# Performance work log

Measured on AMD Instinct MI355X. Metric: run time of the kernel, lower is better.

The kernel has to match this reference:

```python
import jax, jax.numpy as jnp
import numpy as np

B, N, C, H = 8, 2048, 256, 4
RES = 2048
OUT_C = 1


def _split_heads(t, h):
    b, n, hd = t.shape
    return t.reshape(b, n, h, hd // h).transpose(0, 2, 1, 3)


def _merge_heads(t):
    b, h, n, d = t.shape
    return t.transpose(0, 2, 1, 3).reshape(b, n, h * d)


def _inst_norm(x, eps=1e-5):
    # torch InstanceNorm1d applied per-token over head dim, no affine, biased var
    mu = jnp.mean(x, -1, keepdims=True)
    var = jnp.mean((x - mu) ** 2, -1, keepdims=True)
    return (x - mu) / jnp.sqrt(var + eps)


def _layer_norm(x, g, b, eps=1e-5):
    mu = jnp.mean(x, -1, keepdims=True)
    var = jnp.mean((x - mu) ** 2, -1, keepdims=True)
    return (x - mu) / jnp.sqrt(var + eps) * g + b


def _rot_half(x):
    d = x.shape[-1] // 2
    return jnp.concatenate([-x[..., d:], x[..., :d]], axis=-1)


def _rotary_freqs(coords, dim, mult):
    # RotaryEmbedding: t * (scale/min_freq), outer with inv_freq, cat(f, f)
    inv = 1.0 / (10000.0 ** (jnp.arange(0, dim, 2, dtype=jnp.float32) / dim))
    f = (coords * mult)[..., None] * inv  # [..., dim//2]
    return jnp.concatenate([f, f], axis=-1)


def _apply_rot(t, f):
    return t * jnp.cos(f) + _rot_half(t) * jnp.sin(f)


def _gelu(x):
    return jax.nn.gelu(x, approximate=False)


def setup_inputs():
    key = jax.random.key(0)
    ks = jax.random.split(key, 20)
    def rn(k, shp, s=0.02):
        return jax.random.normal(k, shp, dtype=jnp.float32) * s
    return {
        "z": jax.random.normal(ks[0], (B, N, C), jnp.float32),
        "propagate_pos": jax.random.uniform(ks[1], (B, N, 1), jnp.float32),
        # Gaussian Fourier feature matrix (fixed, scale=8)
        "B_fourier": jax.random.normal(ks[2], (1, C), jnp.float32) * 8.0,
        "W_coord": rn(ks[3], (2 * C, C)),
        # CrossLinearAttention (heads=4, dim_head=C, project_query=False)
        "W_kv": rn(ks[4], (C, 2 * H * C)),
        "Wo_ca": rn(ks[5], (H * C, C)),
        "bo_ca": jnp.zeros((C,), jnp.float32),
        # CrossFormer FFN (mlp_dim=C)
        "Wf1": rn(ks[6], (C, C)), "bf1": jnp.zeros((C,), jnp.float32),
        "Wf2": rn(ks[7], (C, C)), "bf2": jnp.zeros((C,), jnp.float32),
        # propagator: LayerNorm + 3-layer GELU MLP (no biases)
        "ln_g": jnp.ones((C,), jnp.float32), "ln_b": jnp.zeros((C,), jnp.float32),
        "P1": rn(ks[8], (C + 1, C)), "P2": rn(ks[9], (C, C)), "P3": rn(ks[10], (C, C)),
        # decode LinearAttention (heads=1, dim_head=C)
        "W_qkv": rn(ks[11], (C, 3 * C)),
        "Wo_da": rn(ks[12], (C, C)), "bo_da": jnp.zeros((C,), jnp.float32),
        # decode FFN
        "ln2_g": jnp.ones((C,), jnp.float32), "ln2_b": jnp.zeros((C,), jnp.float32),
        "D1": rn(ks[13], (C, C)), "D2": rn(ks[14], (C, C // 2)),
        "D3": rn(ks[15], (C // 2, OUT_C)), "b3": jnp.zeros((OUT_C,), jnp.float32),
    }


def reference(z, propagate_pos, B_fourier, W_coord, W_kv, Wo_ca, bo_ca,
              Wf1, bf1, Wf2, bf2, ln_g, ln_b, P1, P2, P3,
              W_qkv, Wo_da, bo_da, ln2_g, ln2_b, D1, D2, D3, b3):
    pos = propagate_pos  # [B, N, 1]
    n = z.shape[1]
    # --- coordinate projection: Gaussian Fourier features -> GELU -> Linear ---
    xp = 2.0 * np.pi * ((pos / 16.0) @ B_fourier)            # [B, N, C]
    feat = jnp.concatenate([jnp.sin(xp), jnp.cos(xp)], -1)   # [B, N, 2C]
    x = _gelu(feat) @ W_coord                                # [B, N, C]
    # --- cross linear attention ('fourier', heads=4, dim_head=C, q unprojected) ---
    k, v = jnp.split(z @ W_kv, 2, axis=-1)
    k = _split_heads(k, H)
    v = _split_heads(v, H)                                   # [B, H, N, C]
    q = jnp.broadcast_to(x[:, None], (x.shape[0], H, n, C))  # repeat query over heads
    q = _inst_norm(q)
    k = _inst_norm(k)
    f = _rotary_freqs(pos[..., 0], C, float(RES))[:, None]   # scale/min_freq = res
    q = _apply_rot(q, f)
    k = _apply_rot(k, f)                                     # z_pos=None -> same freqs
    dots = jnp.einsum('bhnd,bhne->bhde', k, v)               # [B, H, C, C]
    out = jnp.einsum('bhnd,bhde->bhne', q, dots) / n
    x = _merge_heads(out) @ Wo_ca + bo_ca + x
    # --- CrossFormer FFN + residual ---
    x = _gelu(x @ Wf1 + bf1) @ Wf2 + bf2 + x
    # --- propagator: LN, concat(pos/16), 3-layer GELU MLP, residual ---
    h = jnp.concatenate([_layer_norm(x, ln_g, ln_b), pos / 16.0], -1)
    zp = _gelu(_gelu(h @ P1) @ P2) @ P3 + x
    # --- decode: linear self-attention (heads=1, fourier) + FFN ---
    q2, k2, v2 = jnp.split(zp @ W_qkv, 3, axis=-1)           # each [B, N, C]
    q2 = _inst_norm(q2)
    k2 = _inst_norm(k2)
    f2 = _rotary_freqs(pos[..., 0], C, float(RES))
    q2 = _apply_rot(q2, f2)
    k2 = _apply_rot(k2, f2)
    dots2 = jnp.einsum('bnd,bne->bde', k2, v2)               # [B, C, C]
    att = jnp.einsum('bnd,bde->bne', q2, dots2) / n
    zd = att @ Wo_da + bo_da + zp
    h2 = _layer_norm(zd, ln2_g, ln2_b)
    u = _gelu(_gelu(h2 @ D1) @ D2) @ D3 + b3                 # [B, N, OUT_C]
    u = jnp.transpose(u, (0, 2, 1))                          # 'b n (t c) -> b (t c) n', t=1
    return (u, zp)
```

## Files before the change

kernel.cpp:

```cpp
#include <hip/hip_runtime.h>
#include <hip/hip_bf16.h>

using bf16 = __hip_bfloat16;
typedef __attribute__((ext_vector_type(8))) short short8;
typedef __attribute__((ext_vector_type(4))) short short4v;
typedef __attribute__((ext_vector_type(4))) float f32x4;

constexpr int BB = 8;
constexpr int NN = 2048;
constexpr int CC = 256;
constexpr int NTOK = BB * NN;
constexpr float TWO_PI = 6.283185307179586f;
constexpr float LOG2_1E4 = 13.287712379549449f;

__device__ __forceinline__ float gelu_f(float x) {
  return 0.5f * x * (1.0f + erff(x * 0.7071067811865475f));
}

template <int T>
__device__ __forceinline__ void stats_rows(const float (*buf)[CC], float* mu, float* rs, float eps) {
  __syncthreads();
  int w = threadIdx.x >> 6, l = threadIdx.x & 63;
  if (w < T) {
    float s = 0.f, s2 = 0.f;
#pragma unroll
    for (int j = 0; j < 4; ++j) { float v = buf[w][l + 64 * j]; s += v; s2 += v * v; }
#pragma unroll
    for (int o = 32; o; o >>= 1) { s += __shfl_down(s, o); s2 += __shfl_down(s2, o); }
    if (l == 0) {
      float m = s * (1.f / 256.f);
      float var = fmaxf(s2 * (1.f / 256.f) - m * m, 0.f);
      mu[w] = m; rs[w] = rsqrtf(var + eps);
    }
  }
  __syncthreads();
}

#define GLD16(src, dst)                                                       \
  __builtin_amdgcn_global_load_lds(                                           \
      (const __attribute__((address_space(1))) void*)(src),                   \
      (__attribute__((address_space(3))) void*)(dst), 16, 0, 0)

template <int K, int MI>
__device__ __forceinline__ void gemm_core(
    const bf16* __restrict__ Ap, int lda, const bf16* __restrict__ Bp,
    bf16 (&As)[MI * 32 * 64], bf16 (&Bs)[64 * 64], f32x4 (&acc)[MI][2]) {
  const int tid = threadIdx.x;
  const int w = tid >> 6, l = tid & 63;
  const int srow = l >> 3, scol = (l & 7) * 8;
  const int wm = w >> 1, wn = w & 1;
  for (int kt = 0; kt < K; kt += 64) {
#pragma unroll
    for (int i = 0; i < MI; ++i) {
      int r = (w * MI + i) * 8 + srow;
      GLD16(Ap + (long)r * lda + kt + scol, &As[(w * MI + i) * 512 + l * 8]);
    }
#pragma unroll
    for (int i = 0; i < 2; ++i) {
      int r = (w * 2 + i) * 8 + srow;
      GLD16(Bp + (long)r * K + kt + scol, &Bs[(w * 2 + i) * 512 + l * 8]);
    }
    __syncthreads();
    short8 bfr[2][2];
#pragma unroll
    for (int ni = 0; ni < 2; ++ni)
#pragma unroll
      for (int ks = 0; ks < 2; ++ks)
        bfr[ni][ks] = *(const short8*)&Bs[(wn * 32 + ni * 16 + (l & 15)) * 64 + ks * 32 + (l >> 4) * 8];
#pragma unroll
    for (int mi = 0; mi < MI; ++mi) {
#pragma unroll
      for (int ks = 0; ks < 2; ++ks) {
        short8 afr = *(const short8*)&As[(wm * (MI * 16) + mi * 16 + (l & 15)) * 64 + ks * 32 + (l >> 4) * 8];
#pragma unroll
        for (int ni = 0; ni < 2; ++ni)
          acc[mi][ni] = __builtin_amdgcn_mfma_f32_16x16x32_bf16(afr, bfr[ni][ks], acc[mi][ni], 0, 0, 0);
      }
    }
    __syncthreads();
  }
}

enum { E_BF16 = 0, E_BIAS_RESB_BOTH, E_BIAS_GELU, E_BIAS_RES_F32,
       E_RANK1_GELU, E_GELU, E_RES_BOTH };

template <int K, int EPI>
__global__ void __launch_bounds__(256) k_gemm(
    const bf16* __restrict__ A, int lda, const bf16* __restrict__ Bt,
    long bstride, long zstride, int nOffZ,
    const float* __restrict__ bias, const float* __restrict__ res,
    const bf16* __restrict__ resB, const float* __restrict__ rank1,
    const float* __restrict__ pvec,
    float* __restrict__ outF, bf16* __restrict__ outB, int ldo) {
  __shared__ bf16 As[128 * 64];
  __shared__ bf16 Bs[64 * 64];
  const int tid = threadIdx.x;
  const int w = tid >> 6, l = tid & 63;
  const int m0 = blockIdx.y * 128, n0 = blockIdx.x * 64;
  const int bidx = m0 >> 11;
  const bf16* Bp = Bt + (long)bidx * bstride + (long)blockIdx.z * zstride + (long)n0 * K;
  f32x4 acc[4][2] = {};
  gemm_core<K, 4>(A + (long)m0 * lda, lda, Bp, As, Bs, acc);
  const int wm = w >> 1, wn = w & 1;
  const int zoff = blockIdx.z * nOffZ;
#pragma unroll
  for (int mi = 0; mi < 4; ++mi) {
#pragma unroll
    for (int ni = 0; ni < 2; ++ni) {
      const int bcol = n0 + wn * 32 + ni * 16 + (l & 15);
      const int ocol = bcol + zoff;
#pragma unroll
      for (int r = 0; r < 4; ++r) {
        const int row = m0 + wm * 64 + mi * 16 + (l >> 4) * 4 + r;
        float v = acc[mi][ni][r];
        const long oidx = (long)row * ldo + ocol;
        if constexpr (EPI == E_BF16) { outB[oidx] = __float2bfloat16(v); }
        else if constexpr (EPI == E_BIAS_RESB_BOTH) {
          v += bias[bcol] + __bfloat162float(resB[oidx]);
          outF[oidx] = v; outB[oidx] = __float2bfloat16(v);
        } else if constexpr (EPI == E_BIAS_GELU) {
          v = gelu_f(v + bias[bcol]); outB[oidx] = __float2bfloat16(v);
        } else if constexpr (EPI == E_BIAS_RES_F32) {
          v += bias[bcol] + res[oidx]; outF[oidx] = v;
        } else if constexpr (EPI == E_RANK1_GELU) {
          v = gelu_f(v + pvec[row] * rank1[bcol]); outB[oidx] = __float2bfloat16(v);
        } else if constexpr (EPI == E_GELU) {
          v = gelu_f(v); outB[oidx] = __float2bfloat16(v);
        } else {
          v += res[oidx]; outF[oidx] = v; outB[oidx] = __float2bfloat16(v);
        }
      }
    }
  }
}

template <int K>
__global__ void __launch_bounds__(256) k_gemmT(
    const bf16* __restrict__ A, int lda, const bf16* __restrict__ Bt,
    bf16* __restrict__ T0, bf16* __restrict__ T1, int thresh, int matsPerB,
    float* __restrict__ sS, float* __restrict__ sS2) {
  __shared__ union {
    struct { bf16 A[128 * 64]; bf16 B[64 * 64]; } ab;
    bf16 stage[64 * 132];
  } sm;
  const int tid = threadIdx.x;
  const int w = tid >> 6, l = tid & 63;
  const int m0 = blockIdx.y * 128, n0 = blockIdx.x * 64;
  f32x4 acc[4][2] = {};
  gemm_core<K, 4>(A + (long)m0 * lda, lda, Bt + (long)n0 * K, sm.ab.A, sm.ab.B, acc);
  const int wm = w >> 1, wn = w & 1;

  if (n0 < thresh) {
    float sr[16], s2r[16];
#pragma unroll
    for (int mi = 0; mi < 4; ++mi)
#pragma unroll
      for (int r = 0; r < 4; ++r) {
        float v0 = acc[mi][0][r], v1 = acc[mi][1][r];
        sr[mi * 4 + r] = v0 + v1;
        s2r[mi * 4 + r] = v0 * v0 + v1 * v1;
      }
#pragma unroll
    for (int o = 1; o < 16; o <<= 1) {
#pragma unroll
      for (int i = 0; i < 16; ++i) {
        sr[i] += __shfl_xor(sr[i], o);
        s2r[i] += __shfl_xor(s2r[i], o);
      }
    }
    if ((l & 15) == 0) {
      const int head = n0 >> 8;
      const long base = (long)head * 16384 + m0 + wm * 64 + (l >> 4) * 4;
#pragma unroll
      for (int mi = 0; mi < 4; ++mi)
#pragma unroll
        for (int r = 0; r < 4; ++r) {
          atomicAdd(&sS[base + mi * 16 + r], sr[mi * 4 + r]);
          atomicAdd(&sS2[base + mi * 16 + r], s2r[mi * 4 + r]);
        }
    }
  }

#pragma unroll
  for (int mi = 0; mi < 4; ++mi)
#pragma unroll
    for (int ni = 0; ni < 2; ++ni) {
      int c = wn * 32 + ni * 16 + (l & 15);
      int row0 = wm * 64 + mi * 16 + (l >> 4) * 4;
#pragma unroll
      for (int q = 0; q < 2; ++q) {
        bf16 b0 = __float2bfloat16(acc[mi][ni][2 * q]);
        bf16 b1 = __float2bfloat16(acc[mi][ni][2 * q + 1]);
        unsigned u = (unsigned)*(unsigned short*)&b0 |
                     ((unsigned)*(unsigned short*)&b1 << 16);
        *(unsigned*)&sm.stage[c * 132 + row0 + 2 * q] = u;
      }
    }
  __syncthreads();
  const int b = m0 >> 11, nbase = m0 & 2047;
  const int part = (n0 >= thresh) ? 1 : 0;
  const int cT0 = n0 - (part ? thresh : 0);
  bf16* dst = (part ? T1 : T0) + ((long)(b * matsPerB + (cT0 >> 8))) * 524288
            + (long)(cT0 & 255) * 2048;
  const int c = tid >> 2, ns = tid & 3;
  bf16* rowp = dst + (long)c * 2048 + nbase + ns * 32;
#pragma unroll
  for (int j = 0; j < 4; ++j) {
    short4v lo = *(const short4v*)&sm.stage[c * 132 + ns * 32 + j * 8];
    short4v hi = *(const short4v*)&sm.stage[c * 132 + ns * 32 + j * 8 + 4];
    short8 v;
    v[0] = lo[0]; v[1] = lo[1]; v[2] = lo[2]; v[3] = lo[3];
    v[4] = hi[0]; v[5] = hi[1]; v[6] = hi[2]; v[7] = hi[3];
    *(short8*)&rowp[j * 8] = v;
  }
}

template <int MI>
__global__ void __launch_bounds__(256) k_atb2(
    const bf16* __restrict__ A0, const bf16* __restrict__ B0,
    bf16* __restrict__ D0, float scale) {
  __shared__ bf16 As[MI * 32 * 64];
  __shared__ bf16 Bs[64 * 64];
  const int tid = threadIdx.x;
  const int w = tid >> 6, l = tid & 63;
  const int mat = blockIdx.z;
  const int m0 = blockIdx.y * (MI * 32), n0 = blockIdx.x * 64;
  const bf16* Ap = A0 + (long)mat * 524288 + (long)m0 * 2048;
  const bf16* Bp = B0 + (long)mat * 524288 + (long)n0 * 2048;
  f32x4 acc[MI][2] = {};
  gemm_core<2048, MI>(Ap, 2048, Bp, As, Bs, acc);
  bf16* D = D0 + (long)mat * 65536;
  const int wm = w >> 1, wn = w & 1;
#pragma unroll
  for (int mi = 0; mi < MI; ++mi)
#pragma unroll
    for (int ni = 0; ni < 2; ++ni) {
      int col = n0 + wn * 32 + ni * 16 + (l & 15);
#pragma unroll
      for (int r = 0; r < 4; ++r) {
        int row = m0 + wm * (MI * 16) + mi * 16 + (l >> 4) * 4 + r;
        D[(long)row * 256 + col] = __float2bfloat16(acc[mi][ni][r] * scale);
      }
    }
}

__global__ void __launch_bounds__(256) k_rotnorm(
    bf16* __restrict__ Kt, const float* __restrict__ sS, const float* __restrict__ sS2,
    const bf16* __restrict__ csT, int hshift) {
  const int mat = blockIdx.y, c = blockIdx.x;
  const int n = threadIdx.x * 8;
  const int b = mat >> hshift, h = mat & ((1 << hshift) - 1);
  bf16* r0 = Kt + (long)mat * 524288 + (long)c * 2048 + n;
  bf16* r1 = r0 + 128 * 2048;
  const long tok = (long)b * 2048 + n;
  const bf16* cop = csT + ((long)c * 2) * 16384 + tok;
  const bf16* sip = cop + 16384;
  const float* sp = sS + (long)h * 16384 + tok;
  const float* s2p = sS2 + (long)h * 16384 + tok;
  short8 v0 = *(const short8*)r0, v1 = *(const short8*)r1;
  short8 co8 = *(const short8*)cop, si8 = *(const short8*)sip;
  short8 o0, o1;
#pragma unroll
  for (int e = 0; e < 8; ++e) {
    float s = sp[e], s2 = s2p[e];
    float m = s * (1.f / 256.f);
    float r = rsqrtf(fmaxf(s2 * (1.f / 256.f) - m * m, 0.f) + 1e-5f);
    float a = (__uint_as_float(((unsigned)(unsigned short)v0[e]) << 16) - m) * r;
    float bb = (__uint_as_float(((unsigned)(unsigned short)v1[e]) << 16) - m) * r;
    float co = __uint_as_float(((unsigned)(unsigned short)co8[e]) << 16);
    float si = __uint_as_float(((unsigned)(unsigned short)si8[e]) << 16);
    bf16 t0 = __float2bfloat16(a * co - bb * si);
    bf16 t1 = __float2bfloat16(bb * co + a * si);
    o0[e] = *(short*)&t0; o1[e] = *(short*)&t1;
  }
  *(short8*)r0 = o0;
  *(short8*)r1 = o1;
}

__global__ void __launch_bounds__(256) k_rotq(
    const bf16* __restrict__ in, bf16* __restrict__ out, const bf16* __restrict__ cs) {
  __shared__ float xr[4][CC];
  __shared__ float mu[4], rs[4];
  int tid = threadIdx.x;
  long tok0 = (long)blockIdx.x * 4;
#pragma unroll
  for (int t = 0; t < 4; ++t) xr[t][tid] = __bfloat162float(in[(tok0 + t) * 256 + tid]);
  stats_rows<4>(xr, mu, rs, 1e-5f);
  int i = tid & 127;
#pragma unroll
  for (int t = 0; t < 4; ++t) {
    float co = __bfloat162float(cs[(tok0 + t) * 256 + i]);
    float si = __bfloat162float(cs[(tok0 + t) * 256 + 128 + i]);
    float n0 = (xr[t][tid] - mu[t]) * rs[t];
    float n1 = (xr[t][tid ^ 128] - mu[t]) * rs[t];
    float o = (tid < 128) ? (n0 * co - n1 * si) : (n0 * co + n1 * si);
    out[(tok0 + t) * 256 + tid] = __float2bfloat16(o);
  }
}

struct WEnt { const float* s; bf16* d; int K; int N; int blk0; };
struct WTab { WEnt e[12]; };

__global__ void __launch_bounds__(256) k_wprep(WTab t, int nblk_tr,
                                               float* __restrict__ zbuf, int zcnt) {
  int bid = blockIdx.x;
  if (bid >= nblk_tr) {
    int idx = (bid - nblk_tr) * 256 + threadIdx.x;
    if (idx < zcnt) zbuf[idx] = 0.f;
    return;
  }
  int ei = 0;
#pragma unroll
  for (int i = 1; i < 12; ++i)
    if (bid >= t.e[i].blk0) ei = i;
  WEnt e = t.e[ei];
  int local = (bid - e.blk0) * 256 + threadIdx.x;
  if (local < e.K * e.N) {
    int n = local / e.K, k = local - n * e.K;
    e.d[local] = __float2bfloat16(e.s[(long)k * e.N + n]);
  }
}

__global__ void __launch_bounds__(256) k_pre(
    const float* __restrict__ pos, const float* __restrict__ Bf,
    const float* __restrict__ z, const float* __restrict__ P1,
    bf16* __restrict__ gf, bf16* __restrict__ cs, bf16* __restrict__ csT,
    float* __restrict__ pvec, bf16* __restrict__ zb, float* __restrict__ P1L) {
  int tid = threadIdx.x;
  long tok0 = (long)blockIdx.x * 4;
  if (blockIdx.x == 0) P1L[tid] = P1[65536 + tid];
  float p[4];
#pragma unroll
  for (int t = 0; t < 4; ++t) p[t] = pos[tok0 + t];
  if (tid < 4) pvec[tok0 + tid] = p[tid] * 0.0625f;
  float bfc = Bf[tid];
#pragma unroll
  for (int t = 0; t < 4; ++t) {
    float xp = TWO_PI * (p[t] * 0.0625f) * bfc;
    float s, c; sincosf(xp, &s, &c);
    gf[(tok0 + t) * 512 + tid] = __float2bfloat16(gelu_f(s));
    gf[(tok0 + t) * 512 + 256 + tid] = __float2bfloat16(gelu_f(c));
    zb[(tok0 + t) * 256 + tid] = __float2bfloat16(z[(tok0 + t) * 256 + tid]);
  }
  if (tid < 128) {
    float inv = exp2f(-((float)tid * (1.f / 128.f)) * LOG2_1E4);
#pragma unroll
    for (int t = 0; t < 4; ++t) {
      float fh = p[t] * 2048.f * inv;
      float s, c; sincosf(fh, &s, &c);
      bf16 cb = __float2bfloat16(c), sb = __float2bfloat16(s);
      cs[(tok0 + t) * 256 + tid] = cb;
      cs[(tok0 + t) * 256 + 128 + tid] = sb;
      csT[(long)(tid * 2) * 16384 + tok0 + t] = cb;
      csT[(long)(tid * 2 + 1) * 16384 + tok0 + t] = sb;
    }
  }
}

__global__ void __launch_bounds__(256) k_ln(
    const float* __restrict__ xin, const float* __restrict__ g,
    const float* __restrict__ b, bf16* __restrict__ hout) {
  __shared__ float xr[4][CC];
  __shared__ float mu[4], rs[4];
  int tid = threadIdx.x;
  long tok0 = (long)blockIdx.x * 4;
#pragma unroll
  for (int t = 0; t < 4; ++t) xr[t][tid] = xin[(tok0 + t) * 256 + tid];
  stats_rows<4>(xr, mu, rs, 1e-5f);
  float gv = g[tid], bv = b[tid];
#pragma unroll
  for (int t = 0; t < 4; ++t)
    hout[(tok0 + t) * 256 + tid] = __float2bfloat16((xr[t][tid] - mu[t]) * rs[t] * gv + bv);
}

__global__ void __launch_bounds__(256) k_final(
    const bf16* __restrict__ g2, const float* __restrict__ D3,
    const float* __restrict__ b3, float* __restrict__ u) {
  int w = threadIdx.x >> 6, l = threadIdx.x & 63;
  long tok = (long)blockIdx.x * 4 + w;
  float s = __bfloat162float(g2[tok * 128 + l]) * D3[l]
          + __bfloat162float(g2[tok * 128 + 64 + l]) * D3[64 + l];
#pragma unroll
  for (int o = 32; o; o >>= 1) s += __shfl_down(s, o);
  if (l == 0) u[tok] = s + b3[0];
}

extern "C" void kernel_launch(void* const* d_in, const int* in_sizes, int n_in,
                              void* d_out, int out_size, void* d_ws, size_t ws_size,
                              hipStream_t stream) {
  const float* z    = (const float*)d_in[0];
  const float* pos  = (const float*)d_in[1];
  const float* Bf   = (const float*)d_in[2];
  const float* Wc   = (const float*)d_in[3];
  const float* Wkv  = (const float*)d_in[4];
  const float* Woca = (const float*)d_in[5];
  const float* boca = (const float*)d_in[6];
  const float* Wf1  = (const float*)d_in[7];
  const float* bf1  = (const float*)d_in[8];
  const float* Wf2  = (const float*)d_in[9];
  const float* bf2  = (const float*)d_in[10];
  const float* lng  = (const float*)d_in[11];
  const float* lnb  = (const float*)d_in[12];
  const float* P1   = (const float*)d_in[13];
  const float* P2   = (const float*)d_in[14];
  const float* P3   = (const float*)d_in[15];
  const float* Wqkv = (const float*)d_in[16];
  const float* Woda = (const float*)d_in[17];
  const float* boda = (const float*)d_in[18];
  const float* ln2g = (const float*)d_in[19];
  const float* ln2b = (const float*)d_in[20];
  const float* D1   = (const float*)d_in[21];
  const float* D2   = (const float*)d_in[22];
  const float* D3   = (const float*)d_in[23];
  const float* b3   = (const float*)d_in[24];

  float* u  = (float*)d_out;
  float* zp = (float*)d_out + NTOK;

  const long MB = 1048576L;
  char* ws = (char*)d_ws;
  bf16*  cs   = (bf16*)(ws);
  bf16*  csT  = (bf16*)(ws + 8 * MB);
  float* pvec = (float*)(ws + 16 * MB);
  long wo = 16 * MB + 65536;
  bf16* WcT   = (bf16*)(ws + wo);               wo += 262144;
  bf16* WkvT  = (bf16*)(ws + wo);               wo += 1048576;
  bf16* WocaT = (bf16*)(ws + wo);               wo += 524288;
  bf16* Wf1T  = (bf16*)(ws + wo);               wo += 131072;
  bf16* Wf2T  = (bf16*)(ws + wo);               wo += 131072;
  bf16* P1T   = (bf16*)(ws + wo);               wo += 131072;
  bf16* P2T   = (bf16*)(ws + wo);               wo += 131072;
  bf16* P3T   = (bf16*)(ws + wo);               wo += 131072;
  bf16* WqkvT = (bf16*)(ws + wo);               wo += 393216;
  bf16* WodaT = (bf16*)(ws + wo);               wo += 131072;
  bf16* D1T   = (bf16*)(ws + wo);               wo += 131072;
  bf16* D2T   = (bf16*)(ws + wo);               wo += 65536;
  float* P1L  = (float*)(ws + wo);              wo += 1024;
  float* sS   = (float*)(ws + wo);              wo += 5 * 16384 * 4;
  float* sS2  = (float*)(ws + wo);              wo += 5 * 16384 * 4;
  char* AR = ws + 24 * MB;
  bf16*  xb     = (bf16*)(AR);
  bf16*  zb     = (bf16*)(AR + 8 * MB);
  bf16*  gf     = (bf16*)(AR + 48 * MB);
  bf16*  Kt     = (bf16*)(AR + 16 * MB);
  bf16*  Vt     = (bf16*)(AR + 48 * MB);
  bf16*  dotsT  = (bf16*)(AR + 8 * MB);
  bf16*  qrot   = (bf16*)(AR + 16 * MB);
  bf16*  merged = (bf16*)(AR + 24 * MB);
  float* x2     = (float*)(AR + 56 * MB);
  bf16*  x2b    = (bf16*)(AR + 72 * MB);
  bf16*  t1     = (bf16*)(AR + 8 * MB);
  float* x3     = (float*)(AR + 16 * MB);
  bf16*  h      = (bf16*)(AR + 32 * MB);
  bf16*  p1o    = (bf16*)(AR + 40 * MB);
  bf16*  p2o    = (bf16*)(AR + 48 * MB);
  bf16*  zpb    = (bf16*)(AR + 56 * MB);
  bf16*  q2b    = (bf16*)(AR + 64 * MB);
  bf16*  k2t    = (bf16*)(AR + 72 * MB);
  bf16*  v2t    = (bf16*)(AR + 8 * MB);
  bf16*  dots2T = (bf16*)(AR + 16 * MB);
  bf16*  att    = (bf16*)(AR + 24 * MB);
  float* zd     = (float*)(AR + 32 * MB);
  bf16*  h2     = (bf16*)(AR + 8 * MB);
  bf16*  g1     = (bf16*)(AR + 16 * MB);
  bf16*  g2     = (bf16*)(AR + 24 * MB);

  WTab tab;
  int nb = 0;
  auto add = [&](int i, const float* s, bf16* d, int K_, int N_) {
    tab.e[i].s = s; tab.e[i].d = d; tab.e[i].K = K_; tab.e[i].N = N_;
    tab.e[i].blk0 = nb; nb += (K_ * N_) / 256;
  };
  add(0, Wc, WcT, 512, 256);
  add(1, Wkv, WkvT, 256, 2048);
  add(2, Woca, WocaT, 1024, 256);
  add(3, Wf1, Wf1T, 256, 256);
  add(4, Wf2, Wf2T, 256, 256);
  add(5, P1, P1T, 256, 256);
  add(6, P2, P2T, 256, 256);
  add(7, P3, P3T, 256, 256);
  add(8, Wqkv, WqkvT, 256, 768);
  add(9, Woda, WodaT, 256, 256);
  add(10, D1, D1T, 256, 256);
  add(11, D2, D2T, 256, 128);
  const int zcnt = 2 * 5 * 16384;
  const int zblk = (zcnt + 255) / 256;
  k_wprep<<<nb + zblk, 256, 0, stream>>>(tab, nb, sS, zcnt);

  k_pre<<<NTOK / 4, 256, 0, stream>>>(pos, Bf, z, P1, gf, cs, csT, pvec, zb, P1L);
  k_gemm<512, E_BF16><<<dim3(4, 128, 1), 256, 0, stream>>>(
      gf, 512, WcT, 0, 0, 0, nullptr, nullptr, nullptr, nullptr, nullptr, nullptr, xb, 256);
  k_gemmT<256><<<dim3(32, 128), 256, 0, stream>>>(zb, 256, WkvT, Kt, Vt, 1024, 4, sS, sS2);
  k_rotnorm<<<dim3(128, 32), 256, 0, stream>>>(Kt, sS, sS2, csT, 2);
  k_atb2<4><<<dim3(4, 2, 32), 256, 0, stream>>>(Vt, Kt, dotsT, 1.f / 2048.f);
  k_rotq<<<NTOK / 4, 256, 0, stream>>>(xb, qrot, cs);
  k_gemm<256, E_BF16><<<dim3(4, 128, 4), 256, 0, stream>>>(
      qrot, 256, dotsT, 262144L, 65536L, 256, nullptr, nullptr, nullptr, nullptr, nullptr,
      nullptr, merged, 1024);
  k_gemm<1024, E_BIAS_RESB_BOTH><<<dim3(4, 128, 1), 256, 0, stream>>>(
      merged, 1024, WocaT, 0, 0, 0, boca, nullptr, xb, nullptr, nullptr, x2, x2b, 256);
  k_gemm<256, E_BIAS_GELU><<<dim3(4, 128, 1), 256, 0, stream>>>(
      x2b, 256, Wf1T, 0, 0, 0, bf1, nullptr, nullptr, nullptr, nullptr, nullptr, t1, 256);
  k_gemm<256, E_BIAS_RES_F32><<<dim3(4, 128, 1), 256, 0, stream>>>(
      t1, 256, Wf2T, 0, 0, 0, bf2, x2, nullptr, nullptr, nullptr, x3, nullptr, 256);
  k_ln<<<NTOK / 4, 256, 0, stream>>>(x3, lng, lnb, h);
  k_gemm<256, E_RANK1_GELU><<<dim3(4, 128, 1), 256, 0, stream>>>(
      h, 256, P1T, 0, 0, 0, nullptr, nullptr, nullptr, P1L, pvec, nullptr, p1o, 256);
  k_gemm<256, E_GELU><<<dim3(4, 128, 1), 256, 0, stream>>>(
      p1o, 256, P2T, 0, 0, 0, nullptr, nullptr, nullptr, nullptr, nullptr, nullptr, p2o, 256);
  k_gemm<256, E_RES_BOTH><<<dim3(4, 128, 1), 256, 0, stream>>>(
      p2o, 256, P3T, 0, 0, 0, nullptr, x3, nullptr, nullptr, nullptr, zp, zpb, 256);
  k_gemm<256, E_BF16><<<dim3(4, 128, 1), 256, 0, stream>>>(
      zpb, 256, WqkvT, 0, 0, 0, nullptr, nullptr, nullptr, nullptr, nullptr, nullptr, q2b, 256);
  k_gemmT<256><<<dim3(8, 128), 256, 0, stream>>>(zpb, 256, WqkvT + 65536, k2t, v2t, 256, 1,
                                                 sS + 4 * 16384, sS2 + 4 * 16384);
  k_rotq<<<NTOK / 4, 256, 0, stream>>>(q2b, q2b, cs);
  k_rotnorm<<<dim3(128, 8), 256, 0, stream>>>(k2t, sS + 4 * 16384, sS2 + 4 * 16384, csT, 0);
  k_atb2<2><<<dim3(4, 4, 8), 256, 0, stream>>>(v2t, k2t, dots2T, 1.f / 2048.f);
  k_gemm<256, E_BF16><<<dim3(4, 128, 1), 256, 0, stream>>>(
      q2b, 256, dots2T, 65536L, 0, 0, nullptr, nullptr, nullptr, nullptr, nullptr,
      nullptr, att, 256);
  k_gemm<256, E_BIAS_RES_F32><<<dim3(4, 128, 1), 256, 0, stream>>>(
      att, 256, WodaT, 0, 0, 0, boda, zp, nullptr, nullptr, nullptr, zd, nullptr, 256);
  k_ln<<<NTOK / 4, 256, 0, stream>>>(zd, ln2g, ln2b, h2);
  k_gemm<256, E_GELU><<<dim3(4, 128, 1), 256, 0, stream>>>(
      h2, 256, D1T, 0, 0, 0, nullptr, nullptr, nullptr, nullptr, nullptr, nullptr, g1, 256);
  k_gemm<256, E_GELU><<<dim3(2, 128, 1), 256, 0, stream>>>(
      g1, 256, D2T, 0, 0, 0, nullptr, nullptr, nullptr, nullptr, nullptr, nullptr, g2, 128);
  k_final<<<NTOK / 4, 256, 0, stream>>>(g2, D3, b3, u);
}
```

Before: 477.1 us.

## Swizzle GEMM LDS tiles and replace atomic norm stats with stats kernel

The shared GEMM core now XOR-swizzles the 16-byte column chunks of the A and B tiles by row, both when staging through global_load_lds and when reading MFMA fragments. This is meant to cut LDS bank conflicts in every GEMM. Separately, the per-token instance-norm sums are no longer built by atomics in the k_gemmT epilogue. A new k_stats kernel computes mean and rstd from the stored bf16 K, which also drops the zero-fill in k_wprep. The trade is an extra full read of K, and the statistics now come from bf16-rounded values instead of fp32 accumulators.

```diff
diff --git a/kernel.cpp b/kernel.cpp
--- a/kernel.cpp
+++ b/kernel.cpp
@@ -47,7 +47,9 @@
     bf16 (&As)[MI * 32 * 64], bf16 (&Bs)[64 * 64], f32x4 (&acc)[MI][2]) {
   const int tid = threadIdx.x;
   const int w = tid >> 6, l = tid & 63;
-  const int srow = l >> 3, scol = (l & 7) * 8;
+  const int srow = l >> 3;
+  const int scol = ((l & 7) ^ srow) * 8;
+  const int rsw = (l & 7) * 8;
   const int wm = w >> 1, wn = w & 1;
   for (int kt = 0; kt < K; kt += 64) {
 #pragma unroll
@@ -66,12 +68,14 @@
     for (int ni = 0; ni < 2; ++ni)
 #pragma unroll
       for (int ks = 0; ks < 2; ++ks)
-        bfr[ni][ks] = *(const short8*)&Bs[(wn * 32 + ni * 16 + (l & 15)) * 64 + ks * 32 + (l >> 4) * 8];
+        bfr[ni][ks] = *(const short8*)&Bs[(wn * 32 + ni * 16 + (l & 15)) * 64 +
+                                          ((ks * 32 + (l >> 4) * 8) ^ rsw)];
 #pragma unroll
     for (int mi = 0; mi < MI; ++mi) {
 #pragma unroll
       for (int ks = 0; ks < 2; ++ks) {
-        short8 afr = *(const short8*)&As[(wm * (MI * 16) + mi * 16 + (l & 15)) * 64 + ks * 32 + (l >> 4) * 8];
+        short8 afr = *(const short8*)&As[(wm * (MI * 16) + mi * 16 + (l & 15)) * 64 +
+                                         ((ks * 32 + (l >> 4) * 8) ^ rsw)];
 #pragma unroll
         for (int ni = 0; ni < 2; ++ni)
           acc[mi][ni] = __builtin_amdgcn_mfma_f32_16x16x32_bf16(afr, bfr[ni][ks], acc[mi][ni], 0, 0, 0);
@@ -137,8 +141,7 @@
 template <int K>
 __global__ void __launch_bounds__(256) k_gemmT(
     const bf16* __restrict__ A, int lda, const bf16* __restrict__ Bt,
-    bf16* __restrict__ T0, bf16* __restrict__ T1, int thresh, int matsPerB,
-    float* __restrict__ sS, float* __restrict__ sS2) {
+    bf16* __restrict__ T0, bf16* __restrict__ T1, int thresh, int matsPerB) {
   __shared__ union {
     struct { bf16 A[128 * 64]; bf16 B[64 * 64]; } ab;
     bf16 stage[64 * 132];
@@ -149,38 +152,6 @@
   f32x4 acc[4][2] = {};
   gemm_core<K, 4>(A + (long)m0 * lda, lda, Bt + (long)n0 * K, sm.ab.A, sm.ab.B, acc);
   const int wm = w >> 1, wn = w & 1;
-
-  if (n0 < thresh) {
-    float sr[16], s2r[16];
-#pragma unroll
-    for (int mi = 0; mi < 4; ++mi)
-#pragma unroll
-      for (int r = 0; r < 4; ++r) {
-        float v0 = acc[mi][0][r], v1 = acc[mi][1][r];
-        sr[mi * 4 + r] = v0 + v1;
-        s2r[mi * 4 + r] = v0 * v0 + v1 * v1;
-      }
-#pragma unroll
-    for (int o = 1; o < 16; o <<= 1) {
-#pragma unroll
-      for (int i = 0; i < 16; ++i) {
-        sr[i] += __shfl_xor(sr[i], o);
-        s2r[i] += __shfl_xor(s2r[i], o);
-      }
-    }
-    if ((l & 15) == 0) {
-      const int head = n0 >> 8;
-      const long base = (long)head * 16384 + m0 + wm * 64 + (l >> 4) * 4;
-#pragma unroll
-      for (int mi = 0; mi < 4; ++mi)
-#pragma unroll
-        for (int r = 0; r < 4; ++r) {
-          atomicAdd(&sS[base + mi * 16 + r], sr[mi * 4 + r]);
-          atomicAdd(&sS2[base + mi * 16 + r], s2r[mi * 4 + r]);
-        }
-    }
-  }
-
 #pragma unroll
   for (int mi = 0; mi < 4; ++mi)
 #pragma unroll
@@ -244,27 +215,41 @@
     }
 }
 
+__global__ void __launch_bounds__(256) k_stats(
+    const bf16* __restrict__ Kt, float* __restrict__ mu, float* __restrict__ rs) {
+  const int mat = blockIdx.y;
+  const int n = blockIdx.x * 256 + threadIdx.x;
+  const bf16* base = Kt + (long)mat * 524288 + n;
+  float s = 0.f, s2 = 0.f;
+#pragma unroll 4
+  for (int c = 0; c < 256; ++c) {
+    float v = __bfloat162float(base[(long)c * 2048]);
+    s += v; s2 += v * v;
+  }
+  float m = s * (1.f / 256.f);
+  mu[(long)mat * 2048 + n] = m;
+  rs[(long)mat * 2048 + n] = rsqrtf(fmaxf(s2 * (1.f / 256.f) - m * m, 0.f) + 1e-5f);
+}
+
 __global__ void __launch_bounds__(256) k_rotnorm(
-    bf16* __restrict__ Kt, const float* __restrict__ sS, const float* __restrict__ sS2,
+    bf16* __restrict__ Kt, const float* __restrict__ mu, const float* __restrict__ rs,
     const bf16* __restrict__ csT, int hshift) {
   const int mat = blockIdx.y, c = blockIdx.x;
   const int n = threadIdx.x * 8;
-  const int b = mat >> hshift, h = mat & ((1 << hshift) - 1);
+  const int b = mat >> hshift;
   bf16* r0 = Kt + (long)mat * 524288 + (long)c * 2048 + n;
   bf16* r1 = r0 + 128 * 2048;
   const long tok = (long)b * 2048 + n;
   const bf16* cop = csT + ((long)c * 2) * 16384 + tok;
   const bf16* sip = cop + 16384;
-  const float* sp = sS + (long)h * 16384 + tok;
-  const float* s2p = sS2 + (long)h * 16384 + tok;
+  const float* mup = mu + (long)mat * 2048 + n;
+  const float* rsp = rs + (long)mat * 2048 + n;
   short8 v0 = *(const short8*)r0, v1 = *(const short8*)r1;
   short8 co8 = *(const short8*)cop, si8 = *(const short8*)sip;
   short8 o0, o1;
 #pragma unroll
   for (int e = 0; e < 8; ++e) {
-    float s = sp[e], s2 = s2p[e];
-    float m = s * (1.f / 256.f);
-    float r = rsqrtf(fmaxf(s2 * (1.f / 256.f) - m * m, 0.f) + 1e-5f);
+    float m = mup[e], r = rsp[e];
     float a = (__uint_as_float(((unsigned)(unsigned short)v0[e]) << 16) - m) * r;
     float bb = (__uint_as_float(((unsigned)(unsigned short)v1[e]) << 16) - m) * r;
     float co = __uint_as_float(((unsigned)(unsigned short)co8[e]) << 16);
@@ -301,14 +286,8 @@
 struct WEnt { const float* s; bf16* d; int K; int N; int blk0; };
 struct WTab { WEnt e[12]; };
 
-__global__ void __launch_bounds__(256) k_wprep(WTab t, int nblk_tr,
-                                               float* __restrict__ zbuf, int zcnt) {
+__global__ void __launch_bounds__(256) k_wprep(WTab t) {
   int bid = blockIdx.x;
-  if (bid >= nblk_tr) {
-    int idx = (bid - nblk_tr) * 256 + threadIdx.x;
-    if (idx < zcnt) zbuf[idx] = 0.f;
-    return;
-  }
   int ei = 0;
 #pragma unroll
   for (int i = 1; i < 12; ++i)
@@ -436,8 +415,8 @@
   bf16* D1T   = (bf16*)(ws + wo);               wo += 131072;
   bf16* D2T   = (bf16*)(ws + wo);               wo += 65536;
   float* P1L  = (float*)(ws + wo);              wo += 1024;
-  float* sS   = (float*)(ws + wo);              wo += 5 * 16384 * 4;
-  float* sS2  = (float*)(ws + wo);              wo += 5 * 16384 * 4;
+  float* muB  = (float*)(ws + wo);              wo += 32 * 2048 * 4;
+  float* rsB  = (float*)(ws + wo);              wo += 32 * 2048 * 4;
   char* AR = ws + 24 * MB;
   bf16*  xb     = (bf16*)(AR);
   bf16*  zb     = (bf16*)(AR + 8 * MB);
@@ -483,15 +462,14 @@
   add(9, Woda, WodaT, 256, 256);
   add(10, D1, D1T, 256, 256);
   add(11, D2, D2T, 256, 128);
-  const int zcnt = 2 * 5 * 16384;
-  const int zblk = (zcnt + 255) / 256;
-  k_wprep<<<nb + zblk, 256, 0, stream>>>(tab, nb, sS, zcnt);
+  k_wprep<<<nb, 256, 0, stream>>>(tab);
 
   k_pre<<<NTOK / 4, 256, 0, stream>>>(pos, Bf, z, P1, gf, cs, csT, pvec, zb, P1L);
   k_gemm<512, E_BF16><<<dim3(4, 128, 1), 256, 0, stream>>>(
       gf, 512, WcT, 0, 0, 0, nullptr, nullptr, nullptr, nullptr, nullptr, nullptr, xb, 256);
-  k_gemmT<256><<<dim3(32, 128), 256, 0, stream>>>(zb, 256, WkvT, Kt, Vt, 1024, 4, sS, sS2);
-  k_rotnorm<<<dim3(128, 32), 256, 0, stream>>>(Kt, sS, sS2, csT, 2);
+  k_gemmT<256><<<dim3(32, 128), 256, 0, stream>>>(zb, 256, WkvT, Kt, Vt, 1024, 4);
+  k_stats<<<dim3(8, 32), 256, 0, stream>>>(Kt, muB, rsB);
+  k_rotnorm<<<dim3(128, 32), 256, 0, stream>>>(Kt, muB, rsB, csT, 2);
   k_atb2<4><<<dim3(4, 2, 32), 256, 0, stream>>>(Vt, Kt, dotsT, 1.f / 2048.f);
   k_rotq<<<NTOK / 4, 256, 0, stream>>>(xb, qrot, cs);
   k_gemm<256, E_BF16><<<dim3(4, 128, 4), 256, 0, stream>>>(
@@ -512,10 +490,10 @@
       p2o, 256, P3T, 0, 0, 0, nullptr, x3, nullptr, nullptr, nullptr, zp, zpb, 256);
   k_gemm<256, E_BF16><<<dim3(4, 128, 1), 256, 0, stream>>>(
       zpb, 256, WqkvT, 0, 0, 0, nullptr, nullptr, nullptr, nullptr, nullptr, nullptr, q2b, 256);
-  k_gemmT<256><<<dim3(8, 128), 256, 0, stream>>>(zpb, 256, WqkvT + 65536, k2t, v2t, 256, 1,
-                                                 sS + 4 * 16384, sS2 + 4 * 16384);
+  k_gemmT<256><<<dim3(8, 128), 256, 0, stream>>>(zpb, 256, WqkvT + 65536, k2t, v2t, 256, 1);
   k_rotq<<<NTOK / 4, 256, 0, stream>>>(q2b, q2b, cs);
-  k_rotnorm<<<dim3(128, 8), 256, 0, stream>>>(k2t, sS + 4 * 16384, sS2 + 4 * 16384, csT, 0);
+  k_stats<<<dim3(8, 8), 256, 0, stream>>>(k2t, muB, rsB);
+  k_rotnorm<<<dim3(128, 8), 256, 0, stream>>>(k2t, muB, rsB, csT, 0);
   k_atb2<2><<<dim3(4, 4, 8), 256, 0, stream>>>(v2t, k2t, dots2T, 1.f / 2048.f);
   k_gemm<256, E_BF16><<<dim3(4, 128, 1), 256, 0, stream>>>(
       q2b, 256, dots2T, 65536L, 0, 0, nullptr, nullptr, nullptr, nullptr, nullptr,
```

New measurement: 476.6 us. About the same (-0.1%).
